# Kernel optimization log

Measured on AMD Instinct MI355X. Metric: run time of the kernel, lower is better.

Reference implementation:

```python
import jax, jax.numpy as jnp
import numpy as np

V, E, H = 32000, 512, 512
B, T = 64, 512


def lstm_dir(x, W, U, b, reverse=False):
    """Keras-semantics LSTM over [B,T,D] -> (hs [B,T,H], h_last, c_last).
    Gate order i,f,g,o; sigmoid recurrent activation, tanh activation.
    Inference mode: dropout=0.1 is inactive (Keras applies it only in training)."""
    xz = jnp.einsum('btd,dg->btg', x, W) + b  # precompute input projections [B,T,4H]
    if reverse:
        xz = xz[:, ::-1]
    h0 = jnp.zeros((x.shape[0], U.shape[0]), x.dtype)
    c0 = jnp.zeros_like(h0)

    def step(carry, zt):
        h, c = carry
        z = zt + h @ U
        i, f, g, o = jnp.split(z, 4, axis=-1)
        c = jax.nn.sigmoid(f) * c + jax.nn.sigmoid(i) * jnp.tanh(g)
        h = jax.nn.sigmoid(o) * jnp.tanh(c)
        return (h, c), h

    (h_last, c_last), hs = jax.lax.scan(step, (h0, c0), jnp.swapaxes(xz, 0, 1))
    hs = jnp.swapaxes(hs, 0, 1)  # [B,T,H]
    if reverse:
        hs = hs[:, ::-1]  # Keras Bidirectional re-aligns backward outputs in time
    return hs, h_last, c_last


def setup_inputs() -> dict:
    key = jax.random.key(0)
    ks = jax.random.split(key, 14)
    s = lambda fan_in: 1.0 / np.sqrt(fan_in)
    p = {
        'encoderinput': jax.random.randint(ks[0], (B, T), 0, V, dtype=jnp.int32),
        'emb': jax.random.normal(ks[1], (V, E), jnp.float32) * 0.02,
        # layer 1 (input dim E), forward and backward directions
        'W1f': jax.random.normal(ks[2], (E, 4 * H), jnp.float32) * s(E),
        'U1f': jax.random.normal(ks[3], (H, 4 * H), jnp.float32) * s(H),
        'b1f': jnp.zeros((4 * H,), jnp.float32),
        'W1b': jax.random.normal(ks[4], (E, 4 * H), jnp.float32) * s(E),
        'U1b': jax.random.normal(ks[5], (H, 4 * H), jnp.float32) * s(H),
        'b1b': jnp.zeros((4 * H,), jnp.float32),
        # layer 2 (input dim 2H from bidirectional concat)
        'W2f': jax.random.normal(ks[6], (2 * H, 4 * H), jnp.float32) * s(2 * H),
        'U2f': jax.random.normal(ks[7], (H, 4 * H), jnp.float32) * s(H),
        'b2f': jnp.zeros((4 * H,), jnp.float32),
        'W2b': jax.random.normal(ks[8], (2 * H, 4 * H), jnp.float32) * s(2 * H),
        'U2b': jax.random.normal(ks[9], (H, 4 * H), jnp.float32) * s(H),
        'b2b': jnp.zeros((4 * H,), jnp.float32),
    }
    return p


def reference(encoderinput, emb, W1f, U1f, b1f, W1b, U1b, b1b,
              W2f, U2f, b2f, W2b, U2b, b2b):
    x = emb[encoderinput]  # [B,T,E]
    hf1, _, _ = lstm_dir(x, W1f, U1f, b1f, reverse=False)
    hb1, _, _ = lstm_dir(x, W1b, U1b, b1b, reverse=True)
    l1 = jnp.concatenate([hf1, hb1], axis=-1)  # [B,T,2H]
    hf2, fh, fc = lstm_dir(l1, W2f, U2f, b2f, reverse=False)
    hb2, bh, bc = lstm_dir(l1, W2b, U2b, b2b, reverse=True)
    encoder_output = jnp.concatenate([hf2, hb2], axis=-1)  # [B,T,2H]
    state_h = jnp.concatenate([fh, bh], axis=-1)  # [B,2H]
    state_c = jnp.concatenate([fc, bc], axis=-1)  # [B,2H]
    return (encoder_output, state_h, state_c)
```

## Files before the change

kernel.cpp:

```cpp
#include <hip/hip_runtime.h>
#include <math.h>


#define NBLK_LSTM 256

typedef __attribute__((ext_vector_type(8))) short bf16x8;
typedef __attribute__((ext_vector_type(16))) float f32x16;

__device__ __forceinline__ float bf2f(unsigned short u) {
  return __uint_as_float(((unsigned)u) << 16);
}
__device__ __forceinline__ unsigned short f2bf(float f) {
  unsigned u = __float_as_uint(f);
  unsigned r = (u + 0x7FFFu + ((u >> 16) & 1u)) >> 16;
  return (unsigned short)r;
}
__device__ __forceinline__ float fsigmoid(float x) {
  return 1.0f / (1.0f + __expf(-x));
}
__device__ __forceinline__ float ftanh(float x) {
  return 1.0f - 2.0f / (1.0f + __expf(2.0f * x));
}
__device__ __forceinline__ void gload16(const void* g, void* l) {
  __builtin_amdgcn_global_load_lds(
      (const __attribute__((address_space(1))) unsigned int*)g,
      (__attribute__((address_space(3))) unsigned int*)l, 16, 0, 0);
}

__global__ __launch_bounds__(256) void transpose_u(const float* __restrict__ U,
                                                   float* __restrict__ Ut) {
  __shared__ float tile[32][33];
  int kt = blockIdx.x & 15;
  int ct = blockIdx.x >> 4;
  int k0 = kt * 32, c0 = ct * 32;
  int tx = threadIdx.x & 31, ty = threadIdx.x >> 5;
#pragma unroll
  for (int i = 0; i < 32; i += 8)
    tile[ty + i][tx] = U[(size_t)(k0 + ty + i) * 2048 + c0 + tx];
  __syncthreads();
#pragma unroll
  for (int i = 0; i < 32; i += 8)
    Ut[(size_t)(c0 + ty + i) * 512 + k0 + tx] = tile[tx][ty + i];
}

__global__ __launch_bounds__(256) void build_w_panels(
    const float* __restrict__ W, unsigned short* __restrict__ Wh,
    unsigned short* __restrict__ Wl, int KT) {
  __shared__ float tile[32][33];
  const int tid = threadIdx.x;
  int kt = blockIdx.x % KT;
  int ct = blockIdx.x / KT;
  int k0 = kt * 32, c0 = ct * 32;
  int tx = tid & 31, ty = tid >> 5;
#pragma unroll
  for (int i = 0; i < 32; i += 8)
    tile[ty + i][tx] = W[(size_t)(k0 + ty + i) * 2048 + c0 + tx];
  __syncthreads();
  const int t = tid & 127;
  const int cl = t & 31, g = t >> 5;
  const int c = c0 + cl;
  const int rm = c & 127, nt = c >> 7;
  const int slot = g ^ (rm & 3);
  size_t off = (((size_t)(nt * KT + kt) * 128 + rm) << 5) + slot * 8;
  bf16x8 hh, ll;
#pragma unroll
  for (int e = 0; e < 8; e++) {
    float f = tile[g * 8 + e][cl];
    unsigned short h = f2bf(f);
    hh[e] = (short)h;
    ll[e] = (short)f2bf(f - bf2f(h));
  }
  if (tid < 128) *(bf16x8*)(Wh + off) = hh;
  else           *(bf16x8*)(Wl + off) = ll;
}

__global__ __launch_bounds__(256) void build_a1_panels(
    const int* __restrict__ ids, const float* __restrict__ emb,
    unsigned short* __restrict__ Apan) {
  const int tid = threadIdx.x;
  const int l = tid & 63, wv = tid >> 6;
  const int m = blockIdx.x * 4 + wv;
  const float* src = emb + (size_t)ids[m] * 512 + l * 8;
  float4 v0 = *(const float4*)src;
  float4 v1 = *(const float4*)(src + 4);
  float f[8] = {v0.x, v0.y, v0.z, v0.w, v1.x, v1.y, v1.z, v1.w};
  bf16x8 hh;
#pragma unroll
  for (int e = 0; e < 8; e++) hh[e] = (short)f2bf(f[e]);
  const int rm = m & 127, mt = m >> 7;
  const int kt = l >> 2, g = l & 3;
  const int slot = g ^ (rm & 3);
  *(bf16x8*)(Apan + (((size_t)(mt * 16 + kt) * 128 + rm) << 5) + slot * 8) = hh;
}

template <int KT>
__global__ __launch_bounds__(256) void gemm_panel(
    const unsigned short* __restrict__ Apan,
    const unsigned short* __restrict__ WhP,
    const unsigned short* __restrict__ WlP,
    const float* __restrict__ bias,
    unsigned short* __restrict__ C) {
  __shared__ __align__(16) char lds[2][24576];

  const int tid = threadIdx.x;
  const int mt = blockIdx.x & 255;
  const int nt = blockIdx.x >> 8;
  const int l = tid & 63;
  const int wv = tid >> 6;
  const int wm = wv >> 1, wn = wv & 1;

  const char* aSrc = (const char*)(Apan + (size_t)mt * KT * 4096);
  const char* hSrc = (const char*)(WhP + (size_t)nt * KT * 4096);
  const char* lSrc = (const char*)(WlP + (size_t)nt * KT * 4096);
  const int wvo = wv * 1024;
  const int lo16 = l * 16;

  f32x16 acc[2][2];
#pragma unroll
  for (int rb = 0; rb < 2; rb++)
#pragma unroll
    for (int cb = 0; cb < 2; cb++)
#pragma unroll
      for (int r = 0; r < 16; r++) acc[rb][cb][r] = 0.0f;

  auto STAGE = [&](int buf, int t) {
    const char* ga = aSrc + (size_t)t * 8192 + wvo + lo16;
    const char* gh = hSrc + (size_t)t * 8192 + wvo + lo16;
    const char* gl = lSrc + (size_t)t * 8192 + wvo + lo16;
    char* da = &lds[buf][0] + wvo;
    char* dh = &lds[buf][8192] + wvo;
    char* dl = &lds[buf][16384] + wvo;
    gload16(ga, da);
    gload16(ga + 4096, da + 4096);
    gload16(gh, dh);
    gload16(gh + 4096, dh + 4096);
    gload16(gl, dl);
    gload16(gl + 4096, dl + 4096);
  };

  STAGE(0, 0);
  asm volatile("s_waitcnt vmcnt(0)" ::: "memory");
  __syncthreads();

  const int aoff0 = (wm * 64 + (l & 31)) * 64;
  const int woff0 = 8192 + (wn * 64 + (l & 31)) * 64;
  const int gbase = l >> 5;
  const int gx = l & 3;

  for (int t = 0; t < KT; t++) {
    if (t + 1 < KT) STAGE((t + 1) & 1, t + 1);
    const char* lb = lds[t & 1];
#pragma unroll
    for (int ks = 0; ks < 2; ks++) {
      const int slot = (((ks << 1) + gbase) ^ gx) << 4;
      bf16x8 a0 = *(const bf16x8*)(lb + aoff0 + slot);
      bf16x8 a1 = *(const bf16x8*)(lb + aoff0 + 2048 + slot);
      bf16x8 h0 = *(const bf16x8*)(lb + woff0 + slot);
      bf16x8 h1 = *(const bf16x8*)(lb + woff0 + 2048 + slot);
      bf16x8 w0 = *(const bf16x8*)(lb + woff0 + 8192 + slot);
      bf16x8 w1 = *(const bf16x8*)(lb + woff0 + 8192 + 2048 + slot);
      acc[0][0] = __builtin_amdgcn_mfma_f32_32x32x16_bf16(a0, h0, acc[0][0], 0, 0, 0);
      acc[0][1] = __builtin_amdgcn_mfma_f32_32x32x16_bf16(a0, h1, acc[0][1], 0, 0, 0);
      acc[1][0] = __builtin_amdgcn_mfma_f32_32x32x16_bf16(a1, h0, acc[1][0], 0, 0, 0);
      acc[1][1] = __builtin_amdgcn_mfma_f32_32x32x16_bf16(a1, h1, acc[1][1], 0, 0, 0);
      acc[0][0] = __builtin_amdgcn_mfma_f32_32x32x16_bf16(a0, w0, acc[0][0], 0, 0, 0);
      acc[0][1] = __builtin_amdgcn_mfma_f32_32x32x16_bf16(a0, w1, acc[0][1], 0, 0, 0);
      acc[1][0] = __builtin_amdgcn_mfma_f32_32x32x16_bf16(a1, w0, acc[1][0], 0, 0, 0);
      acc[1][1] = __builtin_amdgcn_mfma_f32_32x32x16_bf16(a1, w1, acc[1][1], 0, 0, 0);
    }
    asm volatile("s_waitcnt vmcnt(0)" ::: "memory");
    __syncthreads();
  }

  const int m0 = mt * 128, n0 = nt * 128;
  const float b0 = bias[n0 + wn * 64 + (l & 31)];
  const float b1 = bias[n0 + wn * 64 + 32 + (l & 31)];
#pragma unroll
  for (int rb = 0; rb < 2; rb++) {
    const int rowb = m0 + wm * 64 + rb * 32 + 4 * (l >> 5);
#pragma unroll
    for (int cb = 0; cb < 2; cb++) {
      const int col = n0 + wn * 64 + cb * 32 + (l & 31);
      const float bb = cb ? b1 : b0;
#pragma unroll
      for (int r = 0; r < 16; r++) {
        const int row = rowb + (r & 3) + 8 * (r >> 2);
        C[(size_t)row * 2048 + col] = f2bf(acc[rb][cb][r] + bb);
      }
    }
  }
}

__global__ __launch_bounds__(256, 1) void lstm_fused(
    const unsigned short* __restrict__ xzF,
    const unsigned short* __restrict__ xzB,
    const float* __restrict__ UtF,
    const float* __restrict__ UtB,
    float* __restrict__ outF32,
    unsigned short* __restrict__ outB16,
    float* __restrict__ hbuf,
    float* __restrict__ stateh, float* __restrict__ statec,
    unsigned* __restrict__ bar) {
  __shared__ float p_lds[4][32][36];

  const int tid = threadIdx.x;
  const int bid = blockIdx.x;
  const int dir = bid >> 7;
  const int jg  = (bid & 127) >> 1;
  const int bg  = bid & 1;
  const int grp = dir * 2 + bg;

  const unsigned short* xz = dir ? xzB : xzF;
  const float* Ut = dir ? UtB : UtF;
  char* hbuf_c = (char*)hbuf;

  const int l  = tid & 63;
  const int wv = tid >> 6;

  bf16x8 uh8[8], ul8[8];
  {
    const int c = l & 31;
    const size_t gcol = (size_t)((c >> 3) * 512 + jg * 8 + (c & 7));
#pragma unroll
    for (int ks = 0; ks < 8; ks++) {
      const float* src = Ut + gcol * 512 + (wv * 8 + ks) * 16 + ((l >> 5) << 3);
      bf16x8 hh, ll;
#pragma unroll
      for (int e = 0; e < 8; e++) {
        float f = src[e];
        unsigned short us = f2bf(f);
        hh[e] = (short)us;
        ll[e] = (short)f2bf(f - bf2f(us));
      }
      uh8[ks] = hh;
      ul8[ks] = ll;
    }
  }

  const int ub = tid >> 3;
  const int jl = tid & 7;
  const int b  = bg * 32 + ub;
  const int j  = jg * 8 + jl;

  unsigned* leafArr = bar + grp * 128;
  unsigned* myleaf  = leafArr + (jg & 7) * 16;

  const unsigned short* xzb = xz + (size_t)b * (512 * 2048) + j;

  float creg = 0.0f;
  float zx0, zx1, zx2, zx3;
  {
    const unsigned short* p = xzb + (size_t)(dir ? 511 : 0) * 2048;
    zx0 = bf2f(p[0]); zx1 = bf2f(p[512]);
    zx2 = bf2f(p[1024]); zx3 = bf2f(p[1536]);
  }

  const int aoff = ((wv * 16 + (l >> 5)) * 32 + (l & 31)) * 16;
  const int poff = jg * 512 + ub * 16 + jl * 2;

  const int colp = dir * 512 + j;
  const int p_kt = colp >> 5, p_g = (colp >> 3) & 3, p_e = colp & 7;

  for (int s = 0; s < 512; s++) {
    const int tt = dir ? (511 - s) : s;

    if (s > 0) {
      const char* sb = hbuf_c + (size_t)(grp * 2 + (s & 1)) * 65536;
      bf16x8 ahh[8], ahl[8];
#pragma unroll
      for (int ks = 0; ks < 8; ks++) {
        const char* p = sb + aoff + ks * 1024;
        asm volatile("global_load_dwordx4 %0, %1, off sc0 sc1"
                     : "=v"(ahh[ks]) : "v"(p) : "memory");
        asm volatile("global_load_dwordx4 %0, %1, off sc0 sc1"
                     : "=v"(ahl[ks]) : "v"(p + 32768) : "memory");
      }
      asm volatile("s_waitcnt vmcnt(0)" ::: "memory");
      __builtin_amdgcn_sched_barrier(0);

      f32x16 acc;
#pragma unroll
      for (int r = 0; r < 16; r++) acc[r] = 0.0f;
#pragma unroll
      for (int ks = 0; ks < 8; ks++) {
        acc = __builtin_amdgcn_mfma_f32_32x32x16_bf16(ahh[ks], uh8[ks], acc, 0, 0, 0);
        acc = __builtin_amdgcn_mfma_f32_32x32x16_bf16(ahl[ks], uh8[ks], acc, 0, 0, 0);
        acc = __builtin_amdgcn_mfma_f32_32x32x16_bf16(ahh[ks], ul8[ks], acc, 0, 0, 0);
      }
#pragma unroll
      for (int r = 0; r < 16; r++) {
        const int row = (r & 3) + 8 * (r >> 2) + 4 * (l >> 5);
        p_lds[wv][row][l & 31] = acc[r];
      }
    }
    __syncthreads();

    float h;
    {
      float z0 = zx0, z1 = zx1, z2 = zx2, z3 = zx3;
      if (s > 0) {
#pragma unroll
        for (int w = 0; w < 4; w++) {
          z0 += p_lds[w][ub][jl];
          z1 += p_lds[w][ub][8 + jl];
          z2 += p_lds[w][ub][16 + jl];
          z3 += p_lds[w][ub][24 + jl];
        }
      }
      float si = fsigmoid(z0);
      float sf = fsigmoid(z1);
      float tg = ftanh(z2);
      float so = fsigmoid(z3);
      creg = fmaf(sf, creg, si * tg);
      h = so * ftanh(creg);
    }

    const int m = b * 512 + tt;
    if (s < 511) {
      unsigned short hhs = f2bf(h);
      unsigned short hls = f2bf(h - bf2f(hhs));
      char* db = hbuf_c + (size_t)(grp * 2 + ((s & 1) ^ 1)) * 65536;
      char* pj = db + poff;
      unsigned vh = hhs, vl = hls;
      asm volatile("global_store_short %0, %1, off sc0 sc1"
                   :: "v"(pj), "v"(vh) : "memory");
      asm volatile("global_store_short %0, %1, off sc0 sc1"
                   :: "v"(pj + 32768), "v"(vl) : "memory");
      asm volatile("s_waitcnt vmcnt(0)" ::: "memory");
      __syncthreads();
      if (tid == 0)
        __hip_atomic_fetch_add(myleaf, 1u, __ATOMIC_RELAXED,
                               __HIP_MEMORY_SCOPE_AGENT);
      if (outB16) {
        const int rm = m & 127, mt = m >> 7;
        outB16[(((size_t)(mt * 32 + p_kt) * 128 + rm) << 5) +
               (p_g ^ (rm & 3)) * 8 + p_e] = f2bf(h);
      } else {
        outF32[((size_t)m) * 1024 + colp] = h;
      }
      {
        const int tn = dir ? (510 - s) : (s + 1);
        const unsigned short* p = xzb + (size_t)tn * 2048;
        zx0 = bf2f(p[0]); zx1 = bf2f(p[512]);
        zx2 = bf2f(p[1024]); zx3 = bf2f(p[1536]);
      }
      if (tid < 8) {
        const unsigned tgt = 8u * (unsigned)(s + 1);
        while (__hip_atomic_load(leafArr + tid * 16, __ATOMIC_RELAXED,
                                 __HIP_MEMORY_SCOPE_AGENT) < tgt)
          __builtin_amdgcn_s_sleep(1);
      }
      __syncthreads();
    } else {
      if (outB16) {
        const int rm = m & 127, mt = m >> 7;
        outB16[(((size_t)(mt * 32 + p_kt) * 128 + rm) << 5) +
               (p_g ^ (rm & 3)) * 8 + p_e] = f2bf(h);
      } else {
        outF32[((size_t)m) * 1024 + colp] = h;
      }
      if (stateh != nullptr) {
        stateh[b * 1024 + colp] = h;
        statec[b * 1024 + colp] = creg;
      }
    }
  }
}

extern "C" void kernel_launch(void* const* d_in, const int* in_sizes, int n_in,
                              void* d_out, int out_size, void* d_ws, size_t ws_size,
                              hipStream_t stream) {
  const int*   ids = (const int*)d_in[0];
  const float* emb = (const float*)d_in[1];
  const float* W1f = (const float*)d_in[2];
  const float* U1f = (const float*)d_in[3];
  const float* b1f = (const float*)d_in[4];
  const float* W1b = (const float*)d_in[5];
  const float* U1b = (const float*)d_in[6];
  const float* b1b = (const float*)d_in[7];
  const float* W2f = (const float*)d_in[8];
  const float* U2f = (const float*)d_in[9];
  const float* b2f = (const float*)d_in[10];
  const float* W2b = (const float*)d_in[11];
  const float* U2b = (const float*)d_in[12];
  const float* b2b = (const float*)d_in[13];
  float* out = (float*)d_out;

  char* ws = (char*)d_ws;
  unsigned short* xzF = (unsigned short*)(ws + 0ull);
  unsigned short* xzB = (unsigned short*)(ws + 134217728ull);
  float* Ut1f = (float*)(ws + 268435456ull);
  float* Ut1b = Ut1f + 1048576;
  float* Ut2f = Ut1b + 1048576;
  float* Ut2b = Ut2f + 1048576;
  float* hbuf = (float*)(ws + 285212672ull);
  unsigned* bar = (unsigned*)(ws + 285736960ull);

  char* outc = (char*)d_out;
  unsigned short* l1pan = (unsigned short*)outc;
  unsigned short* A1pan = (unsigned short*)(outc + 67108864ull);
  unsigned short* Wh1f = (unsigned short*)(outc + 100663296ull);
  unsigned short* Wl1f = (unsigned short*)(outc + 102760448ull);
  unsigned short* Wh1b = (unsigned short*)(outc + 104857600ull);
  unsigned short* Wl1b = (unsigned short*)(outc + 106954752ull);
  unsigned short* Wh2f = (unsigned short*)(outc + 109051904ull);
  unsigned short* Wl2f = (unsigned short*)(outc + 113246208ull);
  unsigned short* Wh2b = (unsigned short*)(outc + 117440512ull);
  unsigned short* Wl2b = (unsigned short*)(outc + 121634816ull);

  transpose_u<<<1024, 256, 0, stream>>>(U1f, Ut1f);
  transpose_u<<<1024, 256, 0, stream>>>(U1b, Ut1b);
  transpose_u<<<1024, 256, 0, stream>>>(U2f, Ut2f);
  transpose_u<<<1024, 256, 0, stream>>>(U2b, Ut2b);
  build_w_panels<<<1024, 256, 0, stream>>>(W1f, Wh1f, Wl1f, 16);
  build_w_panels<<<1024, 256, 0, stream>>>(W1b, Wh1b, Wl1b, 16);
  build_w_panels<<<2048, 256, 0, stream>>>(W2f, Wh2f, Wl2f, 32);
  build_w_panels<<<2048, 256, 0, stream>>>(W2b, Wh2b, Wl2b, 32);
  build_a1_panels<<<8192, 256, 0, stream>>>(ids, emb, A1pan);

  gemm_panel<16><<<4096, 256, 0, stream>>>(A1pan, Wh1f, Wl1f, b1f, xzF);
  gemm_panel<16><<<4096, 256, 0, stream>>>(A1pan, Wh1b, Wl1b, b1b, xzB);
  hipMemsetAsync(bar, 0, 4096, stream);
  lstm_fused<<<NBLK_LSTM, 256, 0, stream>>>(xzF, xzB, Ut1f, Ut1b,
                                            nullptr, l1pan, hbuf,
                                            nullptr, nullptr, bar);
  gemm_panel<32><<<4096, 256, 0, stream>>>(l1pan, Wh2f, Wl2f, b2f, xzF);
  gemm_panel<32><<<4096, 256, 0, stream>>>(l1pan, Wh2b, Wl2b, b2b, xzB);
  hipMemsetAsync(bar, 0, 4096, stream);
  lstm_fused<<<NBLK_LSTM, 256, 0, stream>>>(xzF, xzB, Ut2f, Ut2b,
                                            out, nullptr, hbuf,
                                            out + 33554432, out + 33619968, bar);
}
```

Baseline: 4.731 ms.

## Merge fwd/bwd projection GEMMs, drop low-bf16 term in layer 1, restructure LSTM barrier

```diff
diff --git a/kernel.cpp b/kernel.cpp
--- a/kernel.cpp
+++ b/kernel.cpp
@@ -93,21 +93,30 @@
   *(bf16x8*)(Apan + (((size_t)(mt * 16 + kt) * 128 + rm) << 5) + slot * 8) = hh;
 }
 
-template <int KT>
+template <int KT, int TERMS>
 __global__ __launch_bounds__(256) void gemm_panel(
     const unsigned short* __restrict__ Apan,
-    const unsigned short* __restrict__ WhP,
-    const unsigned short* __restrict__ WlP,
-    const float* __restrict__ bias,
-    unsigned short* __restrict__ C) {
+    const unsigned short* __restrict__ WhF,
+    const unsigned short* __restrict__ WlF,
+    const unsigned short* __restrict__ WhB,
+    const unsigned short* __restrict__ WlB,
+    const float* __restrict__ bF, const float* __restrict__ bB,
+    unsigned short* __restrict__ CF, unsigned short* __restrict__ CB) {
   __shared__ __align__(16) char lds[2][24576];
 
   const int tid = threadIdx.x;
-  const int mt = blockIdx.x & 255;
-  const int nt = blockIdx.x >> 8;
+  const int half = blockIdx.x >> 12;
+  const int inner = blockIdx.x & 4095;
+  const int mt = inner & 255;
+  const int nt = inner >> 8;
   const int l = tid & 63;
   const int wv = tid >> 6;
   const int wm = wv >> 1, wn = wv & 1;
+
+  const unsigned short* WhP = half ? WhB : WhF;
+  const unsigned short* WlP = half ? WlB : WlF;
+  const float* bias = half ? bB : bF;
+  unsigned short* C = half ? CB : CF;
 
   const char* aSrc = (const char*)(Apan + (size_t)mt * KT * 4096);
   const char* hSrc = (const char*)(WhP + (size_t)nt * KT * 4096);
@@ -126,16 +135,18 @@
   auto STAGE = [&](int buf, int t) {
     const char* ga = aSrc + (size_t)t * 8192 + wvo + lo16;
     const char* gh = hSrc + (size_t)t * 8192 + wvo + lo16;
-    const char* gl = lSrc + (size_t)t * 8192 + wvo + lo16;
     char* da = &lds[buf][0] + wvo;
     char* dh = &lds[buf][8192] + wvo;
-    char* dl = &lds[buf][16384] + wvo;
     gload16(ga, da);
     gload16(ga + 4096, da + 4096);
     gload16(gh, dh);
     gload16(gh + 4096, dh + 4096);
-    gload16(gl, dl);
-    gload16(gl + 4096, dl + 4096);
+    if (TERMS == 2) {
+      const char* gl = lSrc + (size_t)t * 8192 + wvo + lo16;
+      char* dl = &lds[buf][16384] + wvo;
+      gload16(gl, dl);
+      gload16(gl + 4096, dl + 4096);
+    }
   };
 
   STAGE(0, 0);
@@ -157,16 +168,18 @@
       bf16x8 a1 = *(const bf16x8*)(lb + aoff0 + 2048 + slot);
       bf16x8 h0 = *(const bf16x8*)(lb + woff0 + slot);
       bf16x8 h1 = *(const bf16x8*)(lb + woff0 + 2048 + slot);
-      bf16x8 w0 = *(const bf16x8*)(lb + woff0 + 8192 + slot);
-      bf16x8 w1 = *(const bf16x8*)(lb + woff0 + 8192 + 2048 + slot);
       acc[0][0] = __builtin_amdgcn_mfma_f32_32x32x16_bf16(a0, h0, acc[0][0], 0, 0, 0);
       acc[0][1] = __builtin_amdgcn_mfma_f32_32x32x16_bf16(a0, h1, acc[0][1], 0, 0, 0);
       acc[1][0] = __builtin_amdgcn_mfma_f32_32x32x16_bf16(a1, h0, acc[1][0], 0, 0, 0);
       acc[1][1] = __builtin_amdgcn_mfma_f32_32x32x16_bf16(a1, h1, acc[1][1], 0, 0, 0);
-      acc[0][0] = __builtin_amdgcn_mfma_f32_32x32x16_bf16(a0, w0, acc[0][0], 0, 0, 0);
-      acc[0][1] = __builtin_amdgcn_mfma_f32_32x32x16_bf16(a0, w1, acc[0][1], 0, 0, 0);
-      acc[1][0] = __builtin_amdgcn_mfma_f32_32x32x16_bf16(a1, w0, acc[1][0], 0, 0, 0);
-      acc[1][1] = __builtin_amdgcn_mfma_f32_32x32x16_bf16(a1, w1, acc[1][1], 0, 0, 0);
+      if (TERMS == 2) {
+        bf16x8 w0 = *(const bf16x8*)(lb + woff0 + 8192 + slot);
+        bf16x8 w1 = *(const bf16x8*)(lb + woff0 + 8192 + 2048 + slot);
+        acc[0][0] = __builtin_amdgcn_mfma_f32_32x32x16_bf16(a0, w0, acc[0][0], 0, 0, 0);
+        acc[0][1] = __builtin_amdgcn_mfma_f32_32x32x16_bf16(a0, w1, acc[0][1], 0, 0, 0);
+        acc[1][0] = __builtin_amdgcn_mfma_f32_32x32x16_bf16(a1, w0, acc[1][0], 0, 0, 0);
+        acc[1][1] = __builtin_amdgcn_mfma_f32_32x32x16_bf16(a1, w1, acc[1][1], 0, 0, 0);
+      }
     }
     asm volatile("s_waitcnt vmcnt(0)" ::: "memory");
     __syncthreads();
@@ -201,7 +214,7 @@
     float* __restrict__ hbuf,
     float* __restrict__ stateh, float* __restrict__ statec,
     unsigned* __restrict__ bar) {
-  __shared__ float p_lds[4][32][36];
+  __shared__ float p_lds[2][4][32][36];
 
   const int tid = threadIdx.x;
   const int bid = blockIdx.x;
@@ -265,6 +278,15 @@
     const int tt = dir ? (511 - s) : s;
 
     if (s > 0) {
+      {
+        const unsigned tgt = 8u * (unsigned)s;
+#pragma unroll
+        for (int i = 0; i < 8; i++) {
+          while (__hip_atomic_load(leafArr + i * 16, __ATOMIC_RELAXED,
+                                   __HIP_MEMORY_SCOPE_AGENT) < tgt)
+            __builtin_amdgcn_s_sleep(1);
+        }
+      }
       const char* sb = hbuf_c + (size_t)(grp * 2 + (s & 1)) * 65536;
       bf16x8 ahh[8], ahl[8];
 #pragma unroll
@@ -290,7 +312,7 @@
 #pragma unroll
       for (int r = 0; r < 16; r++) {
         const int row = (r & 3) + 8 * (r >> 2) + 4 * (l >> 5);
-        p_lds[wv][row][l & 31] = acc[r];
+        p_lds[s & 1][wv][row][l & 31] = acc[r];
       }
     }
     __syncthreads();
@@ -301,10 +323,10 @@
       if (s > 0) {
 #pragma unroll
         for (int w = 0; w < 4; w++) {
-          z0 += p_lds[w][ub][jl];
-          z1 += p_lds[w][ub][8 + jl];
-          z2 += p_lds[w][ub][16 + jl];
-          z3 += p_lds[w][ub][24 + jl];
+          z0 += p_lds[s & 1][w][ub][jl];
+          z1 += p_lds[s & 1][w][ub][8 + jl];
+          z2 += p_lds[s & 1][w][ub][16 + jl];
+          z3 += p_lds[s & 1][w][ub][24 + jl];
         }
       }
       float si = fsigmoid(z0);
@@ -326,11 +348,6 @@
                    :: "v"(pj), "v"(vh) : "memory");
       asm volatile("global_store_short %0, %1, off sc0 sc1"
                    :: "v"(pj + 32768), "v"(vl) : "memory");
-      asm volatile("s_waitcnt vmcnt(0)" ::: "memory");
-      __syncthreads();
-      if (tid == 0)
-        __hip_atomic_fetch_add(myleaf, 1u, __ATOMIC_RELAXED,
-                               __HIP_MEMORY_SCOPE_AGENT);
       if (outB16) {
         const int rm = m & 127, mt = m >> 7;
         outB16[(((size_t)(mt * 32 + p_kt) * 128 + rm) << 5) +
@@ -338,19 +355,17 @@
       } else {
         outF32[((size_t)m) * 1024 + colp] = h;
       }
+      asm volatile("s_waitcnt vmcnt(0)" ::: "memory");
+      __syncthreads();
+      if (tid == 0)
+        __hip_atomic_fetch_add(myleaf, 1u, __ATOMIC_RELAXED,
+                               __HIP_MEMORY_SCOPE_AGENT);
       {
         const int tn = dir ? (510 - s) : (s + 1);
         const unsigned short* p = xzb + (size_t)tn * 2048;
         zx0 = bf2f(p[0]); zx1 = bf2f(p[512]);
         zx2 = bf2f(p[1024]); zx3 = bf2f(p[1536]);
       }
-      if (tid < 8) {
-        const unsigned tgt = 8u * (unsigned)(s + 1);
-        while (__hip_atomic_load(leafArr + tid * 16, __ATOMIC_RELAXED,
-                                 __HIP_MEMORY_SCOPE_AGENT) < tgt)
-          __builtin_amdgcn_s_sleep(1);
-      }
-      __syncthreads();
     } else {
       if (outB16) {
         const int rm = m & 127, mt = m >> 7;
@@ -418,14 +433,14 @@
   build_w_panels<<<2048, 256, 0, stream>>>(W2b, Wh2b, Wl2b, 32);
   build_a1_panels<<<8192, 256, 0, stream>>>(ids, emb, A1pan);
 
-  gemm_panel<16><<<4096, 256, 0, stream>>>(A1pan, Wh1f, Wl1f, b1f, xzF);
-  gemm_panel<16><<<4096, 256, 0, stream>>>(A1pan, Wh1b, Wl1b, b1b, xzB);
+  gemm_panel<16, 1><<<8192, 256, 0, stream>>>(A1pan, Wh1f, Wl1f, Wh1b, Wl1b,
+                                              b1f, b1b, xzF, xzB);
   hipMemsetAsync(bar, 0, 4096, stream);
   lstm_fused<<<NBLK_LSTM, 256, 0, stream>>>(xzF, xzB, Ut1f, Ut1b,
                                             nullptr, l1pan, hbuf,
                                             nullptr, nullptr, bar);
-  gemm_panel<32><<<4096, 256, 0, stream>>>(l1pan, Wh2f, Wl2f, b2f, xzF);
-  gemm_panel<32><<<4096, 256, 0, stream>>>(l1pan, Wh2b, Wl2b, b2b, xzB);
+  gemm_panel<32, 2><<<8192, 256, 0, stream>>>(l1pan, Wh2f, Wl2f, Wh2b, Wl2b,
+                                              b2f, b2b, xzF, xzB);
   hipMemsetAsync(bar, 0, 4096, stream);
   lstm_fused<<<NBLK_LSTM, 256, 0, stream>>>(xzF, xzB, Ut2f, Ut2b,
                                             out, nullptr, hbuf,
```

Result: slower. 4.997 ms (+5.6%).
